# Performance work log

Measured on AMD Instinct MI355X. Metric: run time of the kernel, lower is better.

The kernel has to match this reference:

```python
import jax, jax.numpy as jnp
import numpy as np

B, S, W = 32, 256, 32
T = 16               # topics per doc, each spanning L = S//T sentences
VOCAB, E, H, D = 400001, 300, 128, 128


def _gru_scan(x, Wih, Whh, bih, bhh, reverse=False):
    """x: [B,S,E] -> (outputs [B,S,H], final hidden [B,H]). Torch GRU cell math."""
    h0 = jnp.zeros((x.shape[0], Whh.shape[1]), x.dtype)
    gi_all = jnp.einsum('bse,ge->bsg', x, Wih) + bih  # precompute input gates [B,S,3H]

    def step(h, gi):
        gh = h @ Whh.T + bhh
        ir, iz, inn = jnp.split(gi, 3, axis=-1)
        hr, hz, hn = jnp.split(gh, 3, axis=-1)
        r = jax.nn.sigmoid(ir + hr)
        z = jax.nn.sigmoid(iz + hz)
        n = jnp.tanh(inn + r * hn)
        h_new = (1.0 - z) * n + z * h
        return h_new, h_new

    hT, hs = jax.lax.scan(step, h0, jnp.swapaxes(gi_all, 0, 1), reverse=reverse)
    return jnp.swapaxes(hs, 0, 1), hT


def setup_inputs() -> dict:
    key = jax.random.key(0)
    ks = jax.random.split(key, 16)
    sc_i = 1.0 / np.sqrt(H)
    L = S // T
    starts = (jnp.arange(T, dtype=jnp.int32) * L + 1)          # 1-based inclusive
    ends = (jnp.arange(T, dtype=jnp.int32) + 1) * L
    tse = jnp.broadcast_to(jnp.stack([starts, ends], axis=-1)[None], (B, T, 2)).astype(jnp.int32)
    return {
        'word_ids': jax.random.randint(ks[0], (B, S, W), 0, VOCAB, dtype=jnp.int32),
        'topic_start_ends': tse,
        'embed_table': jax.random.normal(ks[1], (VOCAB, E), jnp.float32) * 0.6,
        'Wih_f': jax.random.normal(ks[2], (3 * H, E), jnp.float32) * sc_i,
        'Whh_f': jax.random.normal(ks[3], (3 * H, H), jnp.float32) * sc_i,
        'bih_f': jax.random.normal(ks[4], (3 * H,), jnp.float32) * sc_i,
        'bhh_f': jax.random.normal(ks[5], (3 * H,), jnp.float32) * sc_i,
        'Wih_b': jax.random.normal(ks[6], (3 * H, E), jnp.float32) * sc_i,
        'Whh_b': jax.random.normal(ks[7], (3 * H, H), jnp.float32) * sc_i,
        'bih_b': jax.random.normal(ks[8], (3 * H,), jnp.float32) * sc_i,
        'bhh_b': jax.random.normal(ks[9], (3 * H,), jnp.float32) * sc_i,
        'v_attention': jax.random.normal(ks[10], (4 * H, 1), jnp.float32),
        'W_attention': jax.random.normal(ks[11], (4 * H, 4 * H), jnp.float32) * (1.0 / np.sqrt(4 * H)),
        'W1': jax.random.normal(ks[12], (D, 4 * H), jnp.float32) * (1.0 / np.sqrt(4 * H)),
        'b1': jax.random.normal(ks[13], (D,), jnp.float32) * 0.01,
        'W2': jax.random.normal(ks[14], (1, D), jnp.float32) * (1.0 / np.sqrt(D)),
        'b2': jax.random.normal(ks[15], (1,), jnp.float32) * 0.01,
    }


def reference(word_ids, topic_start_ends, embed_table,
              Wih_f, Whh_f, bih_f, bhh_f, Wih_b, Whh_b, bih_b, bhh_b,
              v_attention, W_attention, W1, b1, W2, b2):
    b, s, _ = word_ids.shape
    h = Whh_f.shape[1]
    # --- sent_encoder: gather word embeddings, mean-pool per sentence ---
    sent_emb = jnp.mean(embed_table[word_ids], axis=2)          # [B,S,E]
    # --- doc_encoder: bi-GRU ---
    out_f, hT_f = _gru_scan(sent_emb, Wih_f, Whh_f, bih_f, bhh_f, reverse=False)
    out_b, hT_b = _gru_scan(sent_emb, Wih_b, Whh_b, bih_b, bhh_b, reverse=True)
    sent_rep = jnp.concatenate([out_f, out_b], axis=-1)         # [B,S,2H]
    # faithful to hidden.view(batch_size, 2H) on hidden of shape [2,B,H]
    doc_vec = jnp.stack([hT_f, hT_b], axis=0).reshape(b, 2 * h)
    doc_rep = jnp.broadcast_to(doc_vec[:, None, :], (b, s, 2 * h))
    # topic reps via segment difference of cumulative GRU states (pad trick)
    pad = jnp.pad(sent_rep, ((0, 0), (1, 1), (0, 0)))           # [B,S+2,2H]
    starts = topic_start_ends[:, :, 0]                          # [B,T], 1-based
    ends = topic_start_ends[:, :, 1]

    def gat(idx, lo, hi):
        return jnp.take_along_axis(pad[..., lo:hi], idx[:, :, None], axis=1)
    fwd_part = gat(ends, 0, h) - gat(starts - 1, 0, h)
    bwd_part = gat(starts, h, 2 * h) - gat(ends + 1, h, 2 * h)
    topic_mat = jnp.concatenate([fwd_part, bwd_part], axis=-1)  # [B,T,2H]
    # scatter topic vectors to sentences: topic id = #starts at or before sentence
    sidx = jnp.arange(s, dtype=starts.dtype)
    topic_id = jnp.sum(sidx[None, :, None] >= (starts - 1)[:, None, :], axis=-1) - 1  # [B,S]
    topic_rep = jnp.take_along_axis(topic_mat, topic_id[:, :, None], axis=1)          # [B,S,2H]
    # --- decoder ---
    cat_ds = jnp.concatenate([doc_rep, sent_rep], axis=-1)      # [B,S,4H]
    cat_ts = jnp.concatenate([topic_rep, sent_rep], axis=-1)
    doc_scores = jnp.tanh(cat_ds @ W_attention) @ v_attention   # [B,S,1]
    topic_scores = jnp.tanh(cat_ts @ W_attention) @ v_attention
    doc_w = jax.nn.softmax(doc_scores, axis=1)
    topic_w = jax.nn.softmax(topic_scores, axis=1)
    context = doc_w * doc_rep + topic_w * topic_rep             # [B,S,2H]
    inp = jnp.concatenate([sent_rep, context], axis=-1)         # [B,S,4H]
    hdd = jax.nn.relu(inp @ W1.T + b1)                          # dropout = identity (eval)
    logits = (hdd @ W2.T + b2).squeeze(-1)                      # [B,S]
    return logits
```

## Files before the change

### kernel.cpp

```cpp
#include <hip/hip_runtime.h>
#include <hip/hip_bf16.h>
#include <cstdint>

#define Bk 32
#define Sk 256
#define Wk 32
#define Tk 16
#define Ek 300
#define Hk 128
#define Dk 128
#define NROWS (Bk*Sk)
#define GI_N  (3*Hk*2)
#define KPAD  320

typedef __attribute__((ext_vector_type(8))) short short8v;
typedef __attribute__((ext_vector_type(4))) float f32x4;

__device__ __forceinline__ float fast_sigmoid(float x) {
    return 1.f / (1.f + __expf(-x));
}
__device__ __forceinline__ float fast_tanh(float x) {
    float ax = fabsf(x);
    float e = __expf(2.f * ax);
    float t = 1.f - 2.f / (1.f + e);
    return copysignf(t, x);
}
__device__ __forceinline__ void barrier_lgkm() {
    asm volatile("s_waitcnt lgkmcnt(0)" ::: "memory");
    __builtin_amdgcn_s_barrier();
}
__device__ __forceinline__ void fma44(const float4& a, const float4& b, float (&c)[4][4]) {
    c[0][0]=fmaf(a.x,b.x,c[0][0]); c[0][1]=fmaf(a.x,b.y,c[0][1]); c[0][2]=fmaf(a.x,b.z,c[0][2]); c[0][3]=fmaf(a.x,b.w,c[0][3]);
    c[1][0]=fmaf(a.y,b.x,c[1][0]); c[1][1]=fmaf(a.y,b.y,c[1][1]); c[1][2]=fmaf(a.y,b.z,c[1][2]); c[1][3]=fmaf(a.y,b.w,c[1][3]);
    c[2][0]=fmaf(a.z,b.x,c[2][0]); c[2][1]=fmaf(a.z,b.y,c[2][1]); c[2][2]=fmaf(a.z,b.z,c[2][2]); c[2][3]=fmaf(a.z,b.w,c[2][3]);
    c[3][0]=fmaf(a.w,b.x,c[3][0]); c[3][1]=fmaf(a.w,b.y,c[3][1]); c[3][2]=fmaf(a.w,b.z,c[3][2]); c[3][3]=fmaf(a.w,b.w,c[3][3]);
}
__device__ __forceinline__ unsigned short f2bf(float f) {
    uint32_t u = __float_as_uint(f);
    uint32_t r = (u + 0x7FFFu + ((u >> 16) & 1u)) >> 16;
    return (unsigned short)r;
}
__device__ __forceinline__ float bf2f(unsigned short h) {
    return __uint_as_float(((uint32_t)h) << 16);
}

__global__ __launch_bounds__(256) void pack_kernel(
    const float* __restrict__ Wf, const float* __restrict__ Wb,
    const float* __restrict__ bf, const float* __restrict__ bb,
    const float* __restrict__ Watt, const float* __restrict__ W1,
    unsigned short* __restrict__ Bgt_hi, unsigned short* __restrict__ Bgt_lo,
    float* __restrict__ bias_gi, unsigned short* __restrict__ Wswt,
    unsigned short* __restrict__ W1H, unsigned short* __restrict__ W1L)
{
    int idx = blockIdx.x * 256 + threadIdx.x;
    if (idx < 768 * KPAD) {
        int n = idx / KPAD, k = idx % KPAD;
        float v = 0.f;
        if (k < 300) v = (n < 384) ? Wf[n * 300 + k] : Wb[(n - 384) * 300 + k];
        unsigned short h = f2bf(v);
        Bgt_hi[idx] = h;
        Bgt_lo[idx] = f2bf(v - bf2f(h));
    }
    if (idx < 768) bias_gi[idx] = (idx < 384) ? bf[idx] : bb[idx - 384];
    if (idx < 512 * 256) {
        int n = idx >> 8, k = idx & 255;
        Wswt[idx] = f2bf(Watt[(size_t)(256 + k) * 512 + n]);
    }
    if (idx < 128 * 512) {
        float v = W1[idx];
        unsigned short h = f2bf(v);
        W1H[idx] = h;
        W1L[idx] = f2bf(v - bf2f(h));
    }
}

__global__ __launch_bounds__(256) void embed_mean_kernel(
    const int* __restrict__ wids, const float* __restrict__ table,
    unsigned short* __restrict__ Ahi, unsigned short* __restrict__ Alo)
{
    int wv = (blockIdx.x << 2) + (threadIdx.x >> 6);
    int lane = threadIdx.x & 63;
    if (wv >= NROWS) return;
    const int* idp = wids + (size_t)wv * Wk;
    float4 a0 = {0,0,0,0}, a1 = {0,0,0,0};
    #pragma unroll 4
    for (int w = 0; w < Wk; ++w) {
        int id = idp[w];
        const float4* r4 = reinterpret_cast<const float4*>(table + (size_t)id * Ek);
        float4 v0 = r4[lane];
        a0.x += v0.x; a0.y += v0.y; a0.z += v0.z; a0.w += v0.w;
        if (lane < 11) {
            float4 v1 = r4[64 + lane];
            a1.x += v1.x; a1.y += v1.y; a1.z += v1.z; a1.w += v1.w;
        }
    }
    const float sc = 1.f / 32.f;
    unsigned short* hp = Ahi + (size_t)wv * KPAD;
    unsigned short* lp = Alo + (size_t)wv * KPAD;
    {
        float v[4] = {a0.x*sc, a0.y*sc, a0.z*sc, a0.w*sc};
        ushort4 h, l;
        h.x=f2bf(v[0]); h.y=f2bf(v[1]); h.z=f2bf(v[2]); h.w=f2bf(v[3]);
        l.x=f2bf(v[0]-bf2f(h.x)); l.y=f2bf(v[1]-bf2f(h.y));
        l.z=f2bf(v[2]-bf2f(h.z)); l.w=f2bf(v[3]-bf2f(h.w));
        *reinterpret_cast<ushort4*>(hp + lane*4) = h;
        *reinterpret_cast<ushort4*>(lp + lane*4) = l;
    }
    if (lane < 11) {
        float v[4] = {a1.x*sc, a1.y*sc, a1.z*sc, a1.w*sc};
        ushort4 h, l;
        h.x=f2bf(v[0]); h.y=f2bf(v[1]); h.z=f2bf(v[2]); h.w=f2bf(v[3]);
        l.x=f2bf(v[0]-bf2f(h.x)); l.y=f2bf(v[1]-bf2f(h.y));
        l.z=f2bf(v[2]-bf2f(h.z)); l.w=f2bf(v[3]-bf2f(h.w));
        *reinterpret_cast<ushort4*>(hp + 256 + lane*4) = h;
        *reinterpret_cast<ushort4*>(lp + 256 + lane*4) = l;
    } else if (lane < 16) {
        ushort4 z = {0,0,0,0};
        *reinterpret_cast<ushort4*>(hp + 256 + lane*4) = z;
        *reinterpret_cast<ushort4*>(lp + 256 + lane*4) = z;
    }
}

template<int PASSES, bool BIAS, bool RELU>
__global__ __launch_bounds__(256) void mfma_gemm_kernel(
    const unsigned short* __restrict__ Ahi, const unsigned short* __restrict__ Alo,
    const unsigned short* __restrict__ Bthi, const unsigned short* __restrict__ Btlo,
    const float* __restrict__ bias, float* __restrict__ C,
    int M, int N, int Kp)
{
    __shared__ unsigned short At_h[128][40];
    __shared__ unsigned short Bt_h[128][40];
    __shared__ unsigned short At_l[128][40];
    __shared__ unsigned short Bt_l[128][40];
    const int tid = threadIdx.x;
    const int m0 = blockIdx.x * 128, n0 = blockIdx.y * 128;
    const int lane = tid & 63;
    const int wave = tid >> 6;
    const int wr = (wave >> 1) * 64, wc = (wave & 1) * 64;
    const int l15 = lane & 15, l4 = lane >> 4;
    f32x4 acc[4][4] = {};

    const int srow = tid >> 1;
    const int scol = (tid & 1) * 16;

    for (int k0 = 0; k0 < Kp; k0 += 32) {
        {
            const unsigned short* ag = Ahi + (size_t)(m0 + srow) * Kp + k0 + scol;
            *reinterpret_cast<short8v*>(&At_h[srow][scol])     = *reinterpret_cast<const short8v*>(ag);
            *reinterpret_cast<short8v*>(&At_h[srow][scol + 8]) = *reinterpret_cast<const short8v*>(ag + 8);
            const unsigned short* bg = Bthi + (size_t)(n0 + srow) * Kp + k0 + scol;
            *reinterpret_cast<short8v*>(&Bt_h[srow][scol])     = *reinterpret_cast<const short8v*>(bg);
            *reinterpret_cast<short8v*>(&Bt_h[srow][scol + 8]) = *reinterpret_cast<const short8v*>(bg + 8);
            if (PASSES > 1) {
                const unsigned short* ag2 = Alo + (size_t)(m0 + srow) * Kp + k0 + scol;
                *reinterpret_cast<short8v*>(&At_l[srow][scol])     = *reinterpret_cast<const short8v*>(ag2);
                *reinterpret_cast<short8v*>(&At_l[srow][scol + 8]) = *reinterpret_cast<const short8v*>(ag2 + 8);
                const unsigned short* bg2 = Btlo + (size_t)(n0 + srow) * Kp + k0 + scol;
                *reinterpret_cast<short8v*>(&Bt_l[srow][scol])     = *reinterpret_cast<const short8v*>(bg2);
                *reinterpret_cast<short8v*>(&Bt_l[srow][scol + 8]) = *reinterpret_cast<const short8v*>(bg2 + 8);
            }
        }
        __syncthreads();
        short8v a_h[4], b_h[4], a_l[4], b_l[4];
        #pragma unroll
        for (int f = 0; f < 4; ++f) {
            a_h[f] = *reinterpret_cast<const short8v*>(&At_h[wr + f*16 + l15][l4*8]);
            b_h[f] = *reinterpret_cast<const short8v*>(&Bt_h[wc + f*16 + l15][l4*8]);
            if (PASSES > 1) {
                a_l[f] = *reinterpret_cast<const short8v*>(&At_l[wr + f*16 + l15][l4*8]);
                b_l[f] = *reinterpret_cast<const short8v*>(&Bt_l[wc + f*16 + l15][l4*8]);
            }
        }
        #pragma unroll
        for (int i = 0; i < 4; ++i) {
            #pragma unroll
            for (int j = 0; j < 4; ++j) {
                acc[i][j] = __builtin_amdgcn_mfma_f32_16x16x32_bf16(a_h[i], b_h[j], acc[i][j], 0, 0, 0);
                if (PASSES > 1) {
                    acc[i][j] = __builtin_amdgcn_mfma_f32_16x16x32_bf16(a_l[i], b_h[j], acc[i][j], 0, 0, 0);
                    acc[i][j] = __builtin_amdgcn_mfma_f32_16x16x32_bf16(a_h[i], b_l[j], acc[i][j], 0, 0, 0);
                }
            }
        }
        __syncthreads();
    }
    #pragma unroll
    for (int i = 0; i < 4; ++i) {
        #pragma unroll
        for (int j = 0; j < 4; ++j) {
            int col = n0 + wc + j * 16 + l15;
            float badd = BIAS ? bias[col] : 0.f;
            #pragma unroll
            for (int r = 0; r < 4; ++r) {
                int row = m0 + wr + i * 16 + l4 * 4 + r;
                float v = acc[i][j][r] + badd;
                if (RELU) v = fmaxf(v, 0.f);
                C[(size_t)row * N + col] = v;
            }
        }
    }
}

__global__ __launch_bounds__(256) void mfma_swscore_kernel(
    const unsigned short* __restrict__ Ahi, const unsigned short* __restrict__ Bthi,
    const float* __restrict__ dptp, const float* __restrict__ vatt,
    const int* __restrict__ tidmap,
    float* __restrict__ dscp, float* __restrict__ tscp)
{
    __shared__ unsigned short At_h[128][40];
    __shared__ unsigned short Bt_h[128][40];
    const int tid = threadIdx.x;
    const int m0 = blockIdx.x * 128, n0 = blockIdx.y * 128;
    const int Kp = 256;
    const int lane = tid & 63;
    const int wave = tid >> 6;
    const int wr = (wave >> 1) * 64, wc = (wave & 1) * 64;
    const int l15 = lane & 15, l4 = lane >> 4;
    f32x4 acc[4][4] = {};

    const int srow = tid >> 1;
    const int scol = (tid & 1) * 16;

    for (int k0 = 0; k0 < Kp; k0 += 32) {
        {
            const unsigned short* ag = Ahi + (size_t)(m0 + srow) * Kp + k0 + scol;
            *reinterpret_cast<short8v*>(&At_h[srow][scol])     = *reinterpret_cast<const short8v*>(ag);
            *reinterpret_cast<short8v*>(&At_h[srow][scol + 8]) = *reinterpret_cast<const short8v*>(ag + 8);
            const unsigned short* bg = Bthi + (size_t)(n0 + srow) * Kp + k0 + scol;
            *reinterpret_cast<short8v*>(&Bt_h[srow][scol])     = *reinterpret_cast<const short8v*>(bg);
            *reinterpret_cast<short8v*>(&Bt_h[srow][scol + 8]) = *reinterpret_cast<const short8v*>(bg + 8);
        }
        __syncthreads();
        short8v a_h[4], b_h[4];
        #pragma unroll
        for (int f = 0; f < 4; ++f) {
            a_h[f] = *reinterpret_cast<const short8v*>(&At_h[wr + f*16 + l15][l4*8]);
            b_h[f] = *reinterpret_cast<const short8v*>(&Bt_h[wc + f*16 + l15][l4*8]);
        }
        #pragma unroll
        for (int i = 0; i < 4; ++i)
            #pragma unroll
            for (int j = 0; j < 4; ++j)
                acc[i][j] = __builtin_amdgcn_mfma_f32_16x16x32_bf16(a_h[i], b_h[j], acc[i][j], 0, 0, 0);
        __syncthreads();
    }
    const int bb = m0 >> 8;
    const float* dpr = dptp + (size_t)bb * 512;
    float vv[4], dpv[4];
    #pragma unroll
    for (int j = 0; j < 4; ++j) {
        int col = n0 + wc + j * 16 + l15;
        vv[j] = vatt[col];
        dpv[j] = dpr[col];
    }
    const int slot = blockIdx.y * 2 + (wc >> 6);
    #pragma unroll
    for (int i = 0; i < 4; ++i) {
        #pragma unroll
        for (int r = 0; r < 4; ++r) {
            int row = m0 + wr + i * 16 + l4 * 4 + r;
            int ti = tidmap[row];
            const float* tpr = dptp + (size_t)(32 + bb * 16 + ti) * 512;
            float sd = 0.f, st = 0.f;
            #pragma unroll
            for (int j = 0; j < 4; ++j) {
                int col = n0 + wc + j * 16 + l15;
                float c = acc[i][j][r];
                sd += fast_tanh(c + dpv[j]) * vv[j];
                st += fast_tanh(c + tpr[col]) * vv[j];
            }
            sd += __shfl_xor(sd, 1); sd += __shfl_xor(sd, 2);
            sd += __shfl_xor(sd, 4); sd += __shfl_xor(sd, 8);
            st += __shfl_xor(st, 1); st += __shfl_xor(st, 2);
            st += __shfl_xor(st, 4); st += __shfl_xor(st, 8);
            if (l15 == 0) {
                dscp[(size_t)row * 8 + slot] = sd;
                tscp[(size_t)row * 8 + slot] = st;
            }
        }
    }
}

template<bool BIAS, bool RELU>
__global__ __launch_bounds__(256) void gemm_kernel(
    const float* __restrict__ A, const float* __restrict__ B,
    const float* __restrict__ bias, float* __restrict__ C,
    int M, int N, int K)
{
    __shared__ float As[64][68];
    __shared__ float Bs[64][68];
    const int tid = threadIdx.x;
    const int m0 = blockIdx.x * 64;
    const int n0 = blockIdx.y * 64;
    const int tx = tid & 15, ty = tid >> 4;
    const int lr = tid >> 2;
    const int lc = tid & 3;
    float acc[4][4] = {};

    for (int k0 = 0; k0 < K; k0 += 64) {
        #pragma unroll
        for (int i = 0; i < 4; ++i) {
            int kk = lc * 4 + i * 16;
            int gm = m0 + lr;
            int gk = k0 + kk;
            float4 v = {0,0,0,0};
            if (gm < M && gk < K)
                v = *reinterpret_cast<const float4*>(A + (size_t)gm * K + gk);
            As[kk+0][lr] = v.x; As[kk+1][lr] = v.y; As[kk+2][lr] = v.z; As[kk+3][lr] = v.w;
        }
        #pragma unroll
        for (int i = 0; i < 4; ++i) {
            int nn = lc * 4 + i * 16;
            int gk = k0 + lr;
            float4 v = {0,0,0,0};
            if (gk < K)
                v = *reinterpret_cast<const float4*>(B + (size_t)gk * N + n0 + nn);
            *reinterpret_cast<float4*>(&Bs[lr][nn]) = v;
        }
        __syncthreads();
        #pragma unroll 8
        for (int k = 0; k < 64; ++k) {
            float4 av = *reinterpret_cast<const float4*>(&As[k][ty*4]);
            float4 bv = *reinterpret_cast<const float4*>(&Bs[k][tx*4]);
            fma44(av, bv, acc);
        }
        __syncthreads();
    }
    #pragma unroll
    for (int r = 0; r < 4; ++r) {
        int row = m0 + ty * 4 + r;
        if (row < M) {
            float4 v = {acc[r][0], acc[r][1], acc[r][2], acc[r][3]};
            if (BIAS) {
                const float* bp = bias + n0 + tx * 4;
                v.x += bp[0]; v.y += bp[1]; v.z += bp[2]; v.w += bp[3];
            }
            if (RELU) {
                v.x = fmaxf(v.x, 0.f); v.y = fmaxf(v.y, 0.f);
                v.z = fmaxf(v.z, 0.f); v.w = fmaxf(v.w, 0.f);
            }
            *reinterpret_cast<float4*>(C + (size_t)row * N + n0 + tx * 4) = v;
        }
    }
}

__global__ __launch_bounds__(512, 1) void gru_scan_kernel(
    const float* __restrict__ gi,
    const float* __restrict__ Whh_f, const float* __restrict__ Whh_b,
    const float* __restrict__ bhh_f, const float* __restrict__ bhh_b,
    float* __restrict__ sent_rep, unsigned short* __restrict__ srh,
    float* __restrict__ hT)
{
    const int blk = blockIdx.x;
    const int dir = blk >> 5;
    const int b   = blk & 31;
    const int t = threadIdx.x;
    const int lane = t & 63;
    const int w_id = t >> 6;
    const int q = lane >> 4;
    const int m = lane & 15;
    const int j = w_id * 16 + m;
    const float* Whh = dir ? Whh_b : Whh_f;
    const float* bhh = dir ? bhh_b : bhh_f;
    __shared__ float hbufA[144];
    __shared__ float hbufB[144];

    const float* wr0 = Whh + (size_t)j * 128 + 32 * q;
    const float* wr1 = wr0 + 128 * 128;
    const float* wr2 = wr0 + 256 * 128;
    float4 wA0 = *reinterpret_cast<const float4*>(wr0 +  0);
    float4 wA1 = *reinterpret_cast<const float4*>(wr0 +  4);
    float4 wA2 = *reinterpret_cast<const float4*>(wr0 +  8);
    float4 wA3 = *reinterpret_cast<const float4*>(wr0 + 12);
    float4 wA4 = *reinterpret_cast<const float4*>(wr0 + 16);
    float4 wA5 = *reinterpret_cast<const float4*>(wr0 + 20);
    float4 wA6 = *reinterpret_cast<const float4*>(wr0 + 24);
    float4 wA7 = *reinterpret_cast<const float4*>(wr0 + 28);
    float4 wB0 = *reinterpret_cast<const float4*>(wr1 +  0);
    float4 wB1 = *reinterpret_cast<const float4*>(wr1 +  4);
    float4 wB2 = *reinterpret_cast<const float4*>(wr1 +  8);
    float4 wB3 = *reinterpret_cast<const float4*>(wr1 + 12);
    float4 wB4 = *reinterpret_cast<const float4*>(wr1 + 16);
    float4 wB5 = *reinterpret_cast<const float4*>(wr1 + 20);
    float4 wB6 = *reinterpret_cast<const float4*>(wr1 + 24);
    float4 wB7 = *reinterpret_cast<const float4*>(wr1 + 28);
    float4 wC0 = *reinterpret_cast<const float4*>(wr2 +  0);
    float4 wC1 = *reinterpret_cast<const float4*>(wr2 +  4);
    float4 wC2 = *reinterpret_cast<const float4*>(wr2 +  8);
    float4 wC3 = *reinterpret_cast<const float4*>(wr2 + 12);
    float4 wC4 = *reinterpret_cast<const float4*>(wr2 + 16);
    float4 wC5 = *reinterpret_cast<const float4*>(wr2 + 20);
    float4 wC6 = *reinterpret_cast<const float4*>(wr2 + 24);
    float4 wC7 = *reinterpret_cast<const float4*>(wr2 + 28);
    const float br = bhh[j];
    const float bz = bhh[128 + j];
    const float bn = bhh[256 + j];

    if (t < 144) { hbufA[t] = 0.f; hbufB[t] = 0.f; }

    const int ji = 36 * (j >> 5) + (j & 31);
    const float* gbase = gi + (size_t)(b * Sk) * GI_N + dir * 384 + j;
    float hold = 0.f;
    float ar = 0.f, az = 0.f, an_ = 0.f;
    float brr = 0.f, bzz = 0.f, bnn = 0.f;
    {
        const long s0 = dir ? (Sk - 1) : 0;
        const long s1 = dir ? (Sk - 2) : 1;
        const float* g0 = gbase + s0 * GI_N;
        ar = g0[0]; az = g0[128]; an_ = g0[256];
        const float* g1 = gbase + s1 * GI_N;
        brr = g1[0]; bzz = g1[128]; bnn = g1[256];
    }
    __syncthreads();

    #define STEP(RD, WR, SEXPR, GR, GZ, GN) { \
        const int s = (SEXPR); \
        const float4* hseg = reinterpret_cast<const float4*>(RD) + 9 * q; \
        float pA = 0.f, pB = 0.f, pC = 0.f; \
        { float4 h4; \
          h4 = hseg[0]; \
          pA=fmaf(wA0.x,h4.x,pA); pA=fmaf(wA0.y,h4.y,pA); pA=fmaf(wA0.z,h4.z,pA); pA=fmaf(wA0.w,h4.w,pA); \
          pB=fmaf(wB0.x,h4.x,pB); pB=fmaf(wB0.y,h4.y,pB); pB=fmaf(wB0.z,h4.z,pB); pB=fmaf(wB0.w,h4.w,pB); \
          pC=fmaf(wC0.x,h4.x,pC); pC=fmaf(wC0.y,h4.y,pC); pC=fmaf(wC0.z,h4.z,pC); pC=fmaf(wC0.w,h4.w,pC); \
          h4 = hseg[1]; \
          pA=fmaf(wA1.x,h4.x,pA); pA=fmaf(wA1.y,h4.y,pA); pA=fmaf(wA1.z,h4.z,pA); pA=fmaf(wA1.w,h4.w,pA); \
          pB=fmaf(wB1.x,h4.x,pB); pB=fmaf(wB1.y,h4.y,pB); pB=fmaf(wB1.z,h4.z,pB); pB=fmaf(wB1.w,h4.w,pB); \
          pC=fmaf(wC1.x,h4.x,pC); pC=fmaf(wC1.y,h4.y,pC); pC=fmaf(wC1.z,h4.z,pC); pC=fmaf(wC1.w,h4.w,pC); \
          h4 = hseg[2]; \
          pA=fmaf(wA2.x,h4.x,pA); pA=fmaf(wA2.y,h4.y,pA); pA=fmaf(wA2.z,h4.z,pA); pA=fmaf(wA2.w,h4.w,pA); \
          pB=fmaf(wB2.x,h4.x,pB); pB=fmaf(wB2.y,h4.y,pB); pB=fmaf(wB2.z,h4.z,pB); pB=fmaf(wB2.w,h4.w,pB); \
          pC=fmaf(wC2.x,h4.x,pC); pC=fmaf(wC2.y,h4.y,pC); pC=fmaf(wC2.z,h4.z,pC); pC=fmaf(wC2.w,h4.w,pC); \
          h4 = hseg[3]; \
          pA=fmaf(wA3.x,h4.x,pA); pA=fmaf(wA3.y,h4.y,pA); pA=fmaf(wA3.z,h4.z,pA); pA=fmaf(wA3.w,h4.w,pA); \
          pB=fmaf(wB3.x,h4.x,pB); pB=fmaf(wB3.y,h4.y,pB); pB=fmaf(wB3.z,h4.z,pB); pB=fmaf(wB3.w,h4.w,pB); \
          pC=fmaf(wC3.x,h4.x,pC); pC=fmaf(wC3.y,h4.y,pC); pC=fmaf(wC3.z,h4.z,pC); pC=fmaf(wC3.w,h4.w,pC); \
          h4 = hseg[4]; \
          pA=fmaf(wA4.x,h4.x,pA); pA=fmaf(wA4.y,h4.y,pA); pA=fmaf(wA4.z,h4.z,pA); pA=fmaf(wA4.w,h4.w,pA); \
          pB=fmaf(wB4.x,h4.x,pB); pB=fmaf(wB4.y,h4.y,pB); pB=fmaf(wB4.z,h4.z,pB); pB=fmaf(wB4.w,h4.w,pB); \
          pC=fmaf(wC4.x,h4.x,pC); pC=fmaf(wC4.y,h4.y,pC); pC=fmaf(wC4.z,h4.z,pC); pC=fmaf(wC4.w,h4.w,pC); \
          h4 = hseg[5]; \
          pA=fmaf(wA5.x,h4.x,pA); pA=fmaf(wA5.y,h4.y,pA); pA=fmaf(wA5.z,h4.z,pA); pA=fmaf(wA5.w,h4.w,pA); \
          pB=fmaf(wB5.x,h4.x,pB); pB=fmaf(wB5.y,h4.y,pB); pB=fmaf(wB5.z,h4.z,pB); pB=fmaf(wB5.w,h4.w,pB); \
          pC=fmaf(wC5.x,h4.x,pC); pC=fmaf(wC5.y,h4.y,pC); pC=fmaf(wC5.z,h4.z,pC); pC=fmaf(wC5.w,h4.w,pC); \
          h4 = hseg[6]; \
          pA=fmaf(wA6.x,h4.x,pA); pA=fmaf(wA6.y,h4.y,pA); pA=fmaf(wA6.z,h4.z,pA); pA=fmaf(wA6.w,h4.w,pA); \
          pB=fmaf(wB6.x,h4.x,pB); pB=fmaf(wB6.y,h4.y,pB); pB=fmaf(wB6.z,h4.z,pB); pB=fmaf(wB6.w,h4.w,pB); \
          pC=fmaf(wC6.x,h4.x,pC); pC=fmaf(wC6.y,h4.y,pC); pC=fmaf(wC6.z,h4.z,pC); pC=fmaf(wC6.w,h4.w,pC); \
          h4 = hseg[7]; \
          pA=fmaf(wA7.x,h4.x,pA); pA=fmaf(wA7.y,h4.y,pA); pA=fmaf(wA7.z,h4.z,pA); pA=fmaf(wA7.w,h4.w,pA); \
          pB=fmaf(wB7.x,h4.x,pB); pB=fmaf(wB7.y,h4.y,pB); pB=fmaf(wB7.z,h4.z,pB); pB=fmaf(wB7.w,h4.w,pB); \
          pC=fmaf(wC7.x,h4.x,pC); pC=fmaf(wC7.y,h4.y,pC); pC=fmaf(wC7.z,h4.z,pC); pC=fmaf(wC7.w,h4.w,pC); } \
        pA += __shfl_xor(pA, 16); pA += __shfl_xor(pA, 32); \
        pB += __shfl_xor(pB, 16); pB += __shfl_xor(pB, 32); \
        pC += __shfl_xor(pC, 16); pC += __shfl_xor(pC, 32); \
        if (q == 0) { \
            float r = fast_sigmoid(GR + pA + br); \
            float z = fast_sigmoid(GZ + pB + bz); \
            float n = fast_tanh(GN + r * (pC + bn)); \
            hold = (1.f - z) * n + z * hold; \
            (WR)[ji] = hold; \
            sent_rep[(size_t)(b * Sk + s) * 256 + dir * 128 + j] = hold; \
            srh[(size_t)(b * Sk + s) * 256 + dir * 128 + j] = f2bf(hold); \
            const long sn = dir ? (long)s - 2 : (long)s + 2;    \
            const float* gp = gbase + sn * GI_N; \
            GR = gp[0]; GZ = gp[128]; GN = gp[256]; \
        } \
        barrier_lgkm(); \
    }

    for (int step = 0; step < Sk; step += 2) {
        STEP(hbufA, hbufB, dir ? (Sk - 1 - step) : step, ar, az, an_);
        STEP(hbufB, hbufA, dir ? (Sk - 2 - step) : (step + 1), brr, bzz, bnn);
    }
    #undef STEP

    if (q == 0) hT[dir * 4096 + b * 128 + j] = hold;
}

__device__ __forceinline__ float4 sr_load_guard(const float* sr, int b, int sidx, int j4) {
    if (sidx < 0 || sidx >= Sk) { float4 z = {0,0,0,0}; return z; }
    return reinterpret_cast<const float4*>(sr)[(size_t)(b * Sk + sidx) * 64 + j4];
}
__global__ __launch_bounds__(64) void prep_kernel(
    const int* __restrict__ tse, const float* __restrict__ sent_rep,
    const float* __restrict__ hT, float* __restrict__ dvtm)
{
    const int b = blockIdx.x;
    const int t = blockIdx.y;
    const int j4 = threadIdx.x;
    if (t == 16) {
        int dir = b >> 4;
        int bb = 2 * (b & 15) + (j4 >> 5);
        int jj4 = j4 & 31;
        float4 v = reinterpret_cast<const float4*>(hT)[dir * 1024 + bb * 32 + jj4];
        reinterpret_cast<float4*>(dvtm)[b * 64 + j4] = v;
    } else {
        int st = tse[b * 32 + t * 2];
        int en = tse[b * 32 + t * 2 + 1];
        float4 va, vb;
        if (j4 < 32) {
            va = sr_load_guard(sent_rep, b, en - 1, j4);
            vb = sr_load_guard(sent_rep, b, st - 2, j4);
        } else {
            va = sr_load_guard(sent_rep, b, st - 1, j4);
            vb = sr_load_guard(sent_rep, b, en, j4);
        }
        float4 v = {va.x - vb.x, va.y - vb.y, va.z - vb.z, va.w - vb.w};
        reinterpret_cast<float4*>(dvtm)[(32 + b * 16 + t) * 64 + j4] = v;
    }
}

__global__ __launch_bounds__(256) void topic_map_kernel(
    const int* __restrict__ tse, int* __restrict__ tidmap)
{
    const int b = blockIdx.x, s = threadIdx.x;
    int ti = 0;
    #pragma unroll
    for (int t = 1; t < 16; ++t) ti += (s >= tse[b * 32 + t * 2] - 1) ? 1 : 0;
    tidmap[b * 256 + s] = ti;
}

__global__ __launch_bounds__(256) void softmax_kernel(
    const float* __restrict__ dscp, const float* __restrict__ tscp,
    float* __restrict__ dsc, float* __restrict__ tsc)
{
    const int b = blockIdx.x, sidx = threadIdx.x;
    const int lane = sidx & 63, wid = sidx >> 6;
    __shared__ float rd[4], rt[4];
    const float4* dp8 = reinterpret_cast<const float4*>(dscp + (size_t)(b * Sk + sidx) * 8);
    const float4* tp8 = reinterpret_cast<const float4*>(tscp + (size_t)(b * Sk + sidx) * 8);
    float4 d0 = dp8[0], d1 = dp8[1], t0 = tp8[0], t1 = tp8[1];
    float d = ((d0.x + d0.y) + (d0.z + d0.w)) + ((d1.x + d1.y) + (d1.z + d1.w));
    float t = ((t0.x + t0.y) + (t0.z + t0.w)) + ((t1.x + t1.y) + (t1.z + t1.w));
    float md = d, mt = t;
    #pragma unroll
    for (int off = 32; off; off >>= 1) {
        md = fmaxf(md, __shfl_xor(md, off));
        mt = fmaxf(mt, __shfl_xor(mt, off));
    }
    if (lane == 0) { rd[wid] = md; rt[wid] = mt; }
    __syncthreads();
    md = fmaxf(fmaxf(rd[0], rd[1]), fmaxf(rd[2], rd[3]));
    mt = fmaxf(fmaxf(rt[0], rt[1]), fmaxf(rt[2], rt[3]));
    float ed = __expf(d - md), et = __expf(t - mt);
    float sd = ed, stt = et;
    #pragma unroll
    for (int off = 32; off; off >>= 1) {
        sd += __shfl_xor(sd, off);
        stt += __shfl_xor(stt, off);
    }
    __syncthreads();
    if (lane == 0) { rd[wid] = sd; rt[wid] = stt; }
    __syncthreads();
    sd = rd[0] + rd[1] + rd[2] + rd[3];
    stt = rt[0] + rt[1] + rt[2] + rt[3];
    dsc[b * Sk + sidx] = ed / sd;
    tsc[b * Sk + sidx] = et / stt;
}

__global__ __launch_bounds__(128) void build_inp_kernel(
    const float* __restrict__ sent_rep, const float* __restrict__ dvtm,
    const float* __restrict__ dw, const float* __restrict__ tw,
    const int* __restrict__ tidmap,
    unsigned short* __restrict__ inpH, unsigned short* __restrict__ inpL)
{
    int row = blockIdx.x;
    int b = row >> 8;
    int f4c = threadIdx.x;
    float4 v;
    if (f4c < 64) {
        v = reinterpret_cast<const float4*>(sent_rep)[(size_t)row * 64 + f4c];
    } else {
        int ti = tidmap[row];
        float dwv = dw[row], twv = tw[row];
        int j4 = f4c - 64;
        float4 dv = reinterpret_cast<const float4*>(dvtm)[b * 64 + j4];
        float4 tm = reinterpret_cast<const float4*>(dvtm)[(32 + b * 16 + ti) * 64 + j4];
        v.x = dwv * dv.x + twv * tm.x;
        v.y = dwv * dv.y + twv * tm.y;
        v.z = dwv * dv.z + twv * tm.z;
        v.w = dwv * dv.w + twv * tm.w;
    }
    ushort4 h, l;
    h.x = f2bf(v.x); h.y = f2bf(v.y); h.z = f2bf(v.z); h.w = f2bf(v.w);
    l.x = f2bf(v.x - bf2f(h.x)); l.y = f2bf(v.y - bf2f(h.y));
    l.z = f2bf(v.z - bf2f(h.z)); l.w = f2bf(v.w - bf2f(h.w));
    *reinterpret_cast<ushort4*>(inpH + (size_t)row * 512 + f4c * 4) = h;
    *reinterpret_cast<ushort4*>(inpL + (size_t)row * 512 + f4c * 4) = l;
}

__global__ __launch_bounds__(256) void logits_kernel(
    const float* __restrict__ hdd, const float* __restrict__ W2,
    const float* __restrict__ b2, float* __restrict__ out)
{
    int row = (blockIdx.x << 2) + (threadIdx.x >> 6);
    int lane = threadIdx.x & 63;
    if (row >= NROWS) return;
    float acc = hdd[(size_t)row * 128 + lane] * W2[lane]
              + hdd[(size_t)row * 128 + 64 + lane] * W2[64 + lane];
    #pragma unroll
    for (int off = 32; off; off >>= 1) acc += __shfl_xor(acc, off);
    if (lane == 0) out[row] = acc + b2[0];
}

extern "C" void kernel_launch(void* const* d_in, const int* in_sizes, int n_in,
                              void* d_out, int out_size, void* d_ws, size_t ws_size,
                              hipStream_t stream)
{
    const int*   wids  = (const int*)d_in[0];
    const int*   tse   = (const int*)d_in[1];
    const float* table = (const float*)d_in[2];
    const float* Wihf  = (const float*)d_in[3];
    const float* Whhf  = (const float*)d_in[4];
    const float* bihf  = (const float*)d_in[5];
    const float* bhhf  = (const float*)d_in[6];
    const float* Wihb  = (const float*)d_in[7];
    const float* Whhb  = (const float*)d_in[8];
    const float* bihb  = (const float*)d_in[9];
    const float* bhhb  = (const float*)d_in[10];
    const float* vatt  = (const float*)d_in[11];
    const float* Watt  = (const float*)d_in[12];
    const float* W1    = (const float*)d_in[13];
    const float* b1    = (const float*)d_in[14];
    const float* W2    = (const float*)d_in[15];
    const float* b2    = (const float*)d_in[16];
    float* ws = (float*)d_ws;
    float* out = (float*)d_out;

    unsigned short* Ahi   = (unsigned short*)(ws + 0);
    unsigned short* Alo   = (unsigned short*)(ws + 1310720);
    float* gi             = ws + 2621440;
    float* sent_rep       = ws + 8912896;
    unsigned short* SRhi  = (unsigned short*)(ws + 11010048);
    float* hT             = ws + 12058624;
    float* dvtm           = ws + 12066816;
    float* dptp           = ws + 12206080;
    float* dsc            = ws + 12484608;
    float* tsc            = ws + 12492800;
    unsigned short* BgtH  = (unsigned short*)(ws + 12500992);
    unsigned short* BgtL  = (unsigned short*)(ws + 12623872);
    float* bias_gi        = ws + 12746752;
    unsigned short* Wswt  = (unsigned short*)(ws + 12747520);
    unsigned short* W1H   = (unsigned short*)(ws + 12813056);
    unsigned short* W1L   = (unsigned short*)(ws + 12845824);
    float* dscp           = ws + 12878592;
    float* tscp           = ws + 12944128;
    int*   tidmap         = (int*)(ws + 13009664);
    unsigned short* inpH  = (unsigned short*)(ws + 0);
    unsigned short* inpL  = (unsigned short*)(ws + 2097152);
    float* hdd            = ws + 4194304;

    if (ws_size < (size_t)13017856 * sizeof(float)) return;

    pack_kernel<<<960, 256, 0, stream>>>(Wihf, Wihb, bihf, bihb, Watt, W1,
                                         BgtH, BgtL, bias_gi, Wswt, W1H, W1L);
    embed_mean_kernel<<<2048, 256, 0, stream>>>(wids, table, Ahi, Alo);
    mfma_gemm_kernel<3, true, false><<<dim3(64, 6), 256, 0, stream>>>(
        Ahi, Alo, BgtH, BgtL, bias_gi, gi, NROWS, 768, KPAD);
    gru_scan_kernel<<<64, 512, 0, stream>>>(gi, Whhf, Whhb, bhhf, bhhb,
                                            sent_rep, SRhi, hT);
    prep_kernel<<<dim3(32, 17), 64, 0, stream>>>(tse, sent_rep, hT, dvtm);
    topic_map_kernel<<<32, 256, 0, stream>>>(tse, tidmap);
    gemm_kernel<false,false><<<dim3(9, 8), 256, 0, stream>>>(dvtm, Watt, nullptr, dptp, 544, 512, 256);
    mfma_swscore_kernel<<<dim3(64, 4), 256, 0, stream>>>(
        SRhi, Wswt, dptp, vatt, tidmap, dscp, tscp);
    softmax_kernel<<<32, 256, 0, stream>>>(dscp, tscp, dsc, tsc);
    build_inp_kernel<<<NROWS, 128, 0, stream>>>(sent_rep, dvtm, dsc, tsc, tidmap, inpH, inpL);
    mfma_gemm_kernel<3, true, true><<<dim3(64, 1), 256, 0, stream>>>(
        inpH, inpL, W1H, W1L, b1, hdd, NROWS, 128, 512);
    logits_kernel<<<2048, 256, 0, stream>>>(hdd, W2, b2, out);
}
```

Baseline: 339.8 us.

## Fuse W1 GEMM with logits, MFMA the topic GEMM, batch GRU output stores

Several changes land together. The W1 MFMA GEMM now computes ReLU, the W2 dot product and b2 in its epilogue, so the hdd buffer and the separate logits kernel are gone. The fp32 FMA GEMM for dvtm×W_attention is replaced by the split-bf16 MFMA GEMM on newly packed operands, and topic_map is folded into prep_kernel. The GRU scan also buffers four steps in registers and stores only from the q==0 lanes, taking global stores off the per-step critical path at the cost of extra registers and a larger workspace.

Result: faster. 332.6 us (median of 2 runs) (-2.1%).

```diff
diff --git a/kernel.cpp b/kernel.cpp
--- a/kernel.cpp
+++ b/kernel.cpp
@@ -29,12 +29,6 @@
     asm volatile("s_waitcnt lgkmcnt(0)" ::: "memory");
     __builtin_amdgcn_s_barrier();
 }
-__device__ __forceinline__ void fma44(const float4& a, const float4& b, float (&c)[4][4]) {
-    c[0][0]=fmaf(a.x,b.x,c[0][0]); c[0][1]=fmaf(a.x,b.y,c[0][1]); c[0][2]=fmaf(a.x,b.z,c[0][2]); c[0][3]=fmaf(a.x,b.w,c[0][3]);
-    c[1][0]=fmaf(a.y,b.x,c[1][0]); c[1][1]=fmaf(a.y,b.y,c[1][1]); c[1][2]=fmaf(a.y,b.z,c[1][2]); c[1][3]=fmaf(a.y,b.w,c[1][3]);
-    c[2][0]=fmaf(a.z,b.x,c[2][0]); c[2][1]=fmaf(a.z,b.y,c[2][1]); c[2][2]=fmaf(a.z,b.z,c[2][2]); c[2][3]=fmaf(a.z,b.w,c[2][3]);
-    c[3][0]=fmaf(a.w,b.x,c[3][0]); c[3][1]=fmaf(a.w,b.y,c[3][1]); c[3][2]=fmaf(a.w,b.z,c[3][2]); c[3][3]=fmaf(a.w,b.w,c[3][3]);
-}
 __device__ __forceinline__ unsigned short f2bf(float f) {
     uint32_t u = __float_as_uint(f);
     uint32_t r = (u + 0x7FFFu + ((u >> 16) & 1u)) >> 16;
@@ -50,7 +44,8 @@
     const float* __restrict__ Watt, const float* __restrict__ W1,
     unsigned short* __restrict__ Bgt_hi, unsigned short* __restrict__ Bgt_lo,
     float* __restrict__ bias_gi, unsigned short* __restrict__ Wswt,
-    unsigned short* __restrict__ W1H, unsigned short* __restrict__ W1L)
+    unsigned short* __restrict__ W1H, unsigned short* __restrict__ W1L,
+    unsigned short* __restrict__ WatTopH, unsigned short* __restrict__ WatTopL)
 {
     int idx = blockIdx.x * 256 + threadIdx.x;
     if (idx < 768 * KPAD) {
@@ -65,6 +60,10 @@
     if (idx < 512 * 256) {
         int n = idx >> 8, k = idx & 255;
         Wswt[idx] = f2bf(Watt[(size_t)(256 + k) * 512 + n]);
+        float v = Watt[(size_t)k * 512 + n];
+        unsigned short h = f2bf(v);
+        WatTopH[idx] = h;
+        WatTopL[idx] = f2bf(v - bf2f(h));
     }
     if (idx < 128 * 512) {
         float v = W1[idx];
@@ -201,6 +200,107 @@
     }
 }
 
+__global__ __launch_bounds__(256) void mfma_w1_logits_kernel(
+    const unsigned short* __restrict__ Ahi, const unsigned short* __restrict__ Alo,
+    const unsigned short* __restrict__ Bthi, const unsigned short* __restrict__ Btlo,
+    const float* __restrict__ b1, const float* __restrict__ W2,
+    const float* __restrict__ b2, float* __restrict__ out)
+{
+    __shared__ unsigned short At_h[128][40];
+    __shared__ unsigned short Bt_h[128][40];
+    __shared__ unsigned short At_l[128][40];
+    __shared__ unsigned short Bt_l[128][40];
+    __shared__ float lpart[128];
+    const int Kp = 512;
+    const int tid = threadIdx.x;
+    const int m0 = blockIdx.x * 128;
+    const int lane = tid & 63;
+    const int wave = tid >> 6;
+    const int wr = (wave >> 1) * 64, wc = (wave & 1) * 64;
+    const int l15 = lane & 15, l4 = lane >> 4;
+    f32x4 acc[4][4] = {};
+
+    const int srow = tid >> 1;
+    const int scol = (tid & 1) * 16;
+
+    for (int k0 = 0; k0 < Kp; k0 += 32) {
+        {
+            const unsigned short* ag = Ahi + (size_t)(m0 + srow) * Kp + k0 + scol;
+            *reinterpret_cast<short8v*>(&At_h[srow][scol])     = *reinterpret_cast<const short8v*>(ag);
+            *reinterpret_cast<short8v*>(&At_h[srow][scol + 8]) = *reinterpret_cast<const short8v*>(ag + 8);
+            const unsigned short* bg = Bthi + (size_t)srow * Kp + k0 + scol;
+            *reinterpret_cast<short8v*>(&Bt_h[srow][scol])     = *reinterpret_cast<const short8v*>(bg);
+            *reinterpret_cast<short8v*>(&Bt_h[srow][scol + 8]) = *reinterpret_cast<const short8v*>(bg + 8);
+            const unsigned short* ag2 = Alo + (size_t)(m0 + srow) * Kp + k0 + scol;
+            *reinterpret_cast<short8v*>(&At_l[srow][scol])     = *reinterpret_cast<const short8v*>(ag2);
+            *reinterpret_cast<short8v*>(&At_l[srow][scol + 8]) = *reinterpret_cast<const short8v*>(ag2 + 8);
+            const unsigned short* bg2 = Btlo + (size_t)srow * Kp + k0 + scol;
+            *reinterpret_cast<short8v*>(&Bt_l[srow][scol])     = *reinterpret_cast<const short8v*>(bg2);
+            *reinterpret_cast<short8v*>(&Bt_l[srow][scol + 8]) = *reinterpret_cast<const short8v*>(bg2 + 8);
+        }
+        __syncthreads();
+        short8v a_h[4], b_h[4], a_l[4], b_l[4];
+        #pragma unroll
+        for (int f = 0; f < 4; ++f) {
+            a_h[f] = *reinterpret_cast<const short8v*>(&At_h[wr + f*16 + l15][l4*8]);
+            b_h[f] = *reinterpret_cast<const short8v*>(&Bt_h[wc + f*16 + l15][l4*8]);
+            a_l[f] = *reinterpret_cast<const short8v*>(&At_l[wr + f*16 + l15][l4*8]);
+            b_l[f] = *reinterpret_cast<const short8v*>(&Bt_l[wc + f*16 + l15][l4*8]);
+        }
+        #pragma unroll
+        for (int i = 0; i < 4; ++i) {
+            #pragma unroll
+            for (int j = 0; j < 4; ++j) {
+                acc[i][j] = __builtin_amdgcn_mfma_f32_16x16x32_bf16(a_h[i], b_h[j], acc[i][j], 0, 0, 0);
+                acc[i][j] = __builtin_amdgcn_mfma_f32_16x16x32_bf16(a_l[i], b_h[j], acc[i][j], 0, 0, 0);
+                acc[i][j] = __builtin_amdgcn_mfma_f32_16x16x32_bf16(a_h[i], b_l[j], acc[i][j], 0, 0, 0);
+            }
+        }
+        __syncthreads();
+    }
+    float b1v[4], w2v[4];
+    #pragma unroll
+    for (int j = 0; j < 4; ++j) {
+        int col = wc + j * 16 + l15;
+        b1v[j] = b1[col];
+        w2v[j] = W2[col];
+    }
+    float lsum[4][4];
+    #pragma unroll
+    for (int i = 0; i < 4; ++i) {
+        #pragma unroll
+        for (int r = 0; r < 4; ++r) {
+            float s = 0.f;
+            #pragma unroll
+            for (int j = 0; j < 4; ++j) {
+                float v = fmaxf(acc[i][j][r] + b1v[j], 0.f);
+                s = fmaf(v, w2v[j], s);
+            }
+            s += __shfl_xor(s, 1); s += __shfl_xor(s, 2);
+            s += __shfl_xor(s, 4); s += __shfl_xor(s, 8);
+            lsum[i][r] = s;
+        }
+    }
+    if (wc == 0 && l15 == 0) {
+        #pragma unroll
+        for (int i = 0; i < 4; ++i)
+            #pragma unroll
+            for (int r = 0; r < 4; ++r)
+                lpart[wr + i * 16 + l4 * 4 + r] = lsum[i][r];
+    }
+    __syncthreads();
+    if (wc == 64 && l15 == 0) {
+        float bb2 = b2[0];
+        #pragma unroll
+        for (int i = 0; i < 4; ++i)
+            #pragma unroll
+            for (int r = 0; r < 4; ++r) {
+                int rl = wr + i * 16 + l4 * 4 + r;
+                out[m0 + rl] = lpart[rl] + lsum[i][r] + bb2;
+            }
+    }
+}
+
 __global__ __launch_bounds__(256) void mfma_swscore_kernel(
     const unsigned short* __restrict__ Ahi, const unsigned short* __restrict__ Bthi,
     const float* __restrict__ dptp, const float* __restrict__ vatt,
@@ -277,69 +377,6 @@
                 dscp[(size_t)row * 8 + slot] = sd;
                 tscp[(size_t)row * 8 + slot] = st;
             }
-        }
-    }
-}
-
-template<bool BIAS, bool RELU>
-__global__ __launch_bounds__(256) void gemm_kernel(
-    const float* __restrict__ A, const float* __restrict__ B,
-    const float* __restrict__ bias, float* __restrict__ C,
-    int M, int N, int K)
-{
-    __shared__ float As[64][68];
-    __shared__ float Bs[64][68];
-    const int tid = threadIdx.x;
-    const int m0 = blockIdx.x * 64;
-    const int n0 = blockIdx.y * 64;
-    const int tx = tid & 15, ty = tid >> 4;
-    const int lr = tid >> 2;
-    const int lc = tid & 3;
-    float acc[4][4] = {};
-
-    for (int k0 = 0; k0 < K; k0 += 64) {
-        #pragma unroll
-        for (int i = 0; i < 4; ++i) {
-            int kk = lc * 4 + i * 16;
-            int gm = m0 + lr;
-            int gk = k0 + kk;
-            float4 v = {0,0,0,0};
-            if (gm < M && gk < K)
-                v = *reinterpret_cast<const float4*>(A + (size_t)gm * K + gk);
-            As[kk+0][lr] = v.x; As[kk+1][lr] = v.y; As[kk+2][lr] = v.z; As[kk+3][lr] = v.w;
-        }
-        #pragma unroll
-        for (int i = 0; i < 4; ++i) {
-            int nn = lc * 4 + i * 16;
-            int gk = k0 + lr;
-            float4 v = {0,0,0,0};
-            if (gk < K)
-                v = *reinterpret_cast<const float4*>(B + (size_t)gk * N + n0 + nn);
-            *reinterpret_cast<float4*>(&Bs[lr][nn]) = v;
-        }
-        __syncthreads();
-        #pragma unroll 8
-        for (int k = 0; k < 64; ++k) {
-            float4 av = *reinterpret_cast<const float4*>(&As[k][ty*4]);
-            float4 bv = *reinterpret_cast<const float4*>(&Bs[k][tx*4]);
-            fma44(av, bv, acc);
-        }
-        __syncthreads();
-    }
-    #pragma unroll
-    for (int r = 0; r < 4; ++r) {
-        int row = m0 + ty * 4 + r;
-        if (row < M) {
-            float4 v = {acc[r][0], acc[r][1], acc[r][2], acc[r][3]};
-            if (BIAS) {
-                const float* bp = bias + n0 + tx * 4;
-                v.x += bp[0]; v.y += bp[1]; v.z += bp[2]; v.w += bp[3];
-            }
-            if (RELU) {
-                v.x = fmaxf(v.x, 0.f); v.y = fmaxf(v.y, 0.f);
-                v.z = fmaxf(v.z, 0.f); v.w = fmaxf(v.w, 0.f);
-            }
-            *reinterpret_cast<float4*>(C + (size_t)row * N + n0 + tx * 4) = v;
         }
     }
 }
@@ -413,7 +450,7 @@
     }
     __syncthreads();
 
-    #define STEP(RD, WR, SEXPR, GR, GZ, GN) { \
+    #define STEP(RD, WR, SEXPR, GR, GZ, GN, SAVE) { \
         const int s = (SEXPR); \
         const float4* hseg = reinterpret_cast<const float4*>(RD) + 9 * q; \
         float pA = 0.f, pB = 0.f, pC = 0.f; \
@@ -459,18 +496,33 @@
             float n = fast_tanh(GN + r * (pC + bn)); \
             hold = (1.f - z) * n + z * hold; \
             (WR)[ji] = hold; \
-            sent_rep[(size_t)(b * Sk + s) * 256 + dir * 128 + j] = hold; \
-            srh[(size_t)(b * Sk + s) * 256 + dir * 128 + j] = f2bf(hold); \
-            const long sn = dir ? (long)s - 2 : (long)s + 2;    \
+            SAVE = hold; \
+            const long sn = dir ? (long)s - 2 : (long)s + 2; \
             const float* gp = gbase + sn * GI_N; \
             GR = gp[0]; GZ = gp[128]; GN = gp[256]; \
         } \
         barrier_lgkm(); \
     }
 
-    for (int step = 0; step < Sk; step += 2) {
-        STEP(hbufA, hbufB, dir ? (Sk - 1 - step) : step, ar, az, an_);
-        STEP(hbufB, hbufA, dir ? (Sk - 2 - step) : (step + 1), brr, bzz, bnn);
+    for (int step = 0; step < Sk; step += 4) {
+        float h0 = 0.f, h1 = 0.f, h2 = 0.f, h3 = 0.f;
+        STEP(hbufA, hbufB, dir ? (Sk - 1 - step) : step,       ar, az, an_, h0);
+        STEP(hbufB, hbufA, dir ? (Sk - 2 - step) : (step + 1), brr, bzz, bnn, h1);
+        STEP(hbufA, hbufB, dir ? (Sk - 3 - step) : (step + 2), ar, az, an_, h2);
+        STEP(hbufB, hbufA, dir ? (Sk - 4 - step) : (step + 3), brr, bzz, bnn, h3);
+        if (q == 0) {
+            const size_t base = (size_t)(b * Sk) * 256 + dir * 128 + j;
+            const int sA = dir ? (Sk - 1 - step) : step;
+            const int d1 = dir ? -1 : 1;
+            sent_rep[base + (size_t)(sA)          * 256] = h0;
+            sent_rep[base + (size_t)(sA + d1)     * 256] = h1;
+            sent_rep[base + (size_t)(sA + 2 * d1) * 256] = h2;
+            sent_rep[base + (size_t)(sA + 3 * d1) * 256] = h3;
+            srh[base + (size_t)(sA)          * 256] = f2bf(h0);
+            srh[base + (size_t)(sA + d1)     * 256] = f2bf(h1);
+            srh[base + (size_t)(sA + 2 * d1) * 256] = f2bf(h2);
+            srh[base + (size_t)(sA + 3 * d1) * 256] = f2bf(h3);
+        }
     }
     #undef STEP
 
@@ -483,17 +535,27 @@
 }
 __global__ __launch_bounds__(64) void prep_kernel(
     const int* __restrict__ tse, const float* __restrict__ sent_rep,
-    const float* __restrict__ hT, float* __restrict__ dvtm)
+    const float* __restrict__ hT, float* __restrict__ dvtm,
+    unsigned short* __restrict__ dvtmH, unsigned short* __restrict__ dvtmL,
+    int* __restrict__ tidmap)
 {
     const int b = blockIdx.x;
     const int t = blockIdx.y;
     const int j4 = threadIdx.x;
+    float4 v;
+    int row;
     if (t == 16) {
         int dir = b >> 4;
         int bb = 2 * (b & 15) + (j4 >> 5);
         int jj4 = j4 & 31;
-        float4 v = reinterpret_cast<const float4*>(hT)[dir * 1024 + bb * 32 + jj4];
-        reinterpret_cast<float4*>(dvtm)[b * 64 + j4] = v;
+        v = reinterpret_cast<const float4*>(hT)[dir * 1024 + bb * 32 + jj4];
+        row = b;
+        for (int ss = j4; ss < 256; ss += 64) {
+            int ti = 0;
+            #pragma unroll
+            for (int tt = 1; tt < 16; ++tt) ti += (ss >= tse[b * 32 + tt * 2] - 1) ? 1 : 0;
+            tidmap[b * 256 + ss] = ti;
+        }
     } else {
         int st = tse[b * 32 + t * 2];
         int en = tse[b * 32 + t * 2 + 1];
@@ -505,19 +567,16 @@
             va = sr_load_guard(sent_rep, b, st - 1, j4);
             vb = sr_load_guard(sent_rep, b, en, j4);
         }
-        float4 v = {va.x - vb.x, va.y - vb.y, va.z - vb.z, va.w - vb.w};
-        reinterpret_cast<float4*>(dvtm)[(32 + b * 16 + t) * 64 + j4] = v;
-    }
-}
-
-__global__ __launch_bounds__(256) void topic_map_kernel(
-    const int* __restrict__ tse, int* __restrict__ tidmap)
-{
-    const int b = blockIdx.x, s = threadIdx.x;
-    int ti = 0;
-    #pragma unroll
-    for (int t = 1; t < 16; ++t) ti += (s >= tse[b * 32 + t * 2] - 1) ? 1 : 0;
-    tidmap[b * 256 + s] = ti;
+        v.x = va.x - vb.x; v.y = va.y - vb.y; v.z = va.z - vb.z; v.w = va.w - vb.w;
+        row = 32 + b * 16 + t;
+    }
+    reinterpret_cast<float4*>(dvtm)[row * 64 + j4] = v;
+    ushort4 h, l;
+    h.x = f2bf(v.x); h.y = f2bf(v.y); h.z = f2bf(v.z); h.w = f2bf(v.w);
+    l.x = f2bf(v.x - bf2f(h.x)); l.y = f2bf(v.y - bf2f(h.y));
+    l.z = f2bf(v.z - bf2f(h.z)); l.w = f2bf(v.w - bf2f(h.w));
+    *reinterpret_cast<ushort4*>(dvtmH + (size_t)row * 256 + j4 * 4) = h;
+    *reinterpret_cast<ushort4*>(dvtmL + (size_t)row * 256 + j4 * 4) = l;
 }
 
 __global__ __launch_bounds__(256) void softmax_kernel(
@@ -587,20 +646,6 @@
     l.z = f2bf(v.z - bf2f(h.z)); l.w = f2bf(v.w - bf2f(h.w));
     *reinterpret_cast<ushort4*>(inpH + (size_t)row * 512 + f4c * 4) = h;
     *reinterpret_cast<ushort4*>(inpL + (size_t)row * 512 + f4c * 4) = l;
-}
-
-__global__ __launch_bounds__(256) void logits_kernel(
-    const float* __restrict__ hdd, const float* __restrict__ W2,
-    const float* __restrict__ b2, float* __restrict__ out)
-{
-    int row = (blockIdx.x << 2) + (threadIdx.x >> 6);
-    int lane = threadIdx.x & 63;
-    if (row >= NROWS) return;
-    float acc = hdd[(size_t)row * 128 + lane] * W2[lane]
-              + hdd[(size_t)row * 128 + 64 + lane] * W2[64 + lane];
-    #pragma unroll
-    for (int off = 32; off; off >>= 1) acc += __shfl_xor(acc, off);
-    if (lane == 0) out[row] = acc + b2[0];
 }
 
 extern "C" void kernel_launch(void* const* d_in, const int* in_sizes, int n_in,
@@ -635,38 +680,42 @@
     float* hT             = ws + 12058624;
     float* dvtm           = ws + 12066816;
     float* dptp           = ws + 12206080;
-    float* dsc            = ws + 12484608;
-    float* tsc            = ws + 12492800;
-    unsigned short* BgtH  = (unsigned short*)(ws + 12500992);
-    unsigned short* BgtL  = (unsigned short*)(ws + 12623872);
-    float* bias_gi        = ws + 12746752;
-    unsigned short* Wswt  = (unsigned short*)(ws + 12747520);
-    unsigned short* W1H   = (unsigned short*)(ws + 12813056);
-    unsigned short* W1L   = (unsigned short*)(ws + 12845824);
-    float* dscp           = ws + 12878592;
-    float* tscp           = ws + 12944128;
-    int*   tidmap         = (int*)(ws + 13009664);
+    float* dsc            = ws + 12533760;
+    float* tsc            = ws + 12541952;
+    unsigned short* BgtH  = (unsigned short*)(ws + 12550144);
+    unsigned short* BgtL  = (unsigned short*)(ws + 12673024);
+    float* bias_gi        = ws + 12795904;
+    unsigned short* Wswt  = (unsigned short*)(ws + 12796672);
+    unsigned short* W1H   = (unsigned short*)(ws + 12862208);
+    unsigned short* W1L   = (unsigned short*)(ws + 12894976);
+    float* dscp           = ws + 12927744;
+    float* tscp           = ws + 12993280;
+    int*   tidmap         = (int*)(ws + 13058816);
+    unsigned short* dvtmH = (unsigned short*)(ws + 13067008);
+    unsigned short* dvtmL = (unsigned short*)(ws + 13148928);
+    unsigned short* WatTH = (unsigned short*)(ws + 13230848);
+    unsigned short* WatTL = (unsigned short*)(ws + 13296384);
     unsigned short* inpH  = (unsigned short*)(ws + 0);
     unsigned short* inpL  = (unsigned short*)(ws + 2097152);
-    float* hdd            = ws + 4194304;
-
-    if (ws_size < (size_t)13017856 * sizeof(float)) return;
+
+    if (ws_size < (size_t)13361920 * sizeof(float)) return;
 
     pack_kernel<<<960, 256, 0, stream>>>(Wihf, Wihb, bihf, bihb, Watt, W1,
-                                         BgtH, BgtL, bias_gi, Wswt, W1H, W1L);
+                                         BgtH, BgtL, bias_gi, Wswt, W1H, W1L,
+                                         WatTH, WatTL);
     embed_mean_kernel<<<2048, 256, 0, stream>>>(wids, table, Ahi, Alo);
     mfma_gemm_kernel<3, true, false><<<dim3(64, 6), 256, 0, stream>>>(
         Ahi, Alo, BgtH, BgtL, bias_gi, gi, NROWS, 768, KPAD);
     gru_scan_kernel<<<64, 512, 0, stream>>>(gi, Whhf, Whhb, bhhf, bhhb,
                                             sent_rep, SRhi, hT);
-    prep_kernel<<<dim3(32, 17), 64, 0, stream>>>(tse, sent_rep, hT, dvtm);
-    topic_map_kernel<<<32, 256, 0, stream>>>(tse, tidmap);
-    gemm_kernel<false,false><<<dim3(9, 8), 256, 0, stream>>>(dvtm, Watt, nullptr, dptp, 544, 512, 256);
+    prep_kernel<<<dim3(32, 17), 64, 0, stream>>>(tse, sent_rep, hT, dvtm,
+                                                 dvtmH, dvtmL, tidmap);
+    mfma_gemm_kernel<3, false, false><<<dim3(5, 4), 256, 0, stream>>>(
+        dvtmH, dvtmL, WatTH, WatTL, nullptr, dptp, 640, 512, 256);
     mfma_swscore_kernel<<<dim3(64, 4), 256, 0, stream>>>(
         SRhi, Wswt, dptp, vatt, tidmap, dscp, tscp);
     softmax_kernel<<<32, 256, 0, stream>>>(dscp, tscp, dsc, tsc);
     build_inp_kernel<<<NROWS, 128, 0, stream>>>(sent_rep, dvtm, dsc, tsc, tidmap, inpH, inpL);
-    mfma_gemm_kernel<3, true, true><<<dim3(64, 1), 256, 0, stream>>>(
-        inpH, inpL, W1H, W1L, b1, hdd, NROWS, 128, 512);
-    logits_kernel<<<2048, 256, 0, stream>>>(hdd, W2, b2, out);
-}
+    mfma_w1_logits_kernel<<<dim3(64, 1), 256, 0, stream>>>(
+        inpH, inpL, W1H, W1L, b1, W2, b2, out);
+}
```
